# Kernel tuning notes

Measured on AMD Instinct MI355X. Metric: run time of the kernel, lower is better.

Reference implementation:

```python
import jax, jax.numpy as jnp
import numpy as np

B, NPG, C = 16, 4096, 256          # graphs, nodes per graph per type, feat dim
N = B * NPG                        # nodes per type
E = N * 16                         # edges per edge type (avg degree 16)
RATIO = 0.25
K = int(np.ceil(RATIO * NPG))      # top-k nodes per graph per type


def setup_inputs() -> dict:
    key = jax.random.key(0)
    ks = jax.random.split(key, 16)
    s = 1.0 / np.sqrt(C)
    inp = {
        "x_inst": jax.random.normal(ks[0], (N, C), jnp.float32),
        "x_data": jax.random.normal(ks[1], (N, C), jnp.float32),
        "w_kqv_inst": jax.random.normal(ks[2], (C, 3), jnp.float32) * s,
        "b_kqv_inst": jnp.zeros((3,), jnp.float32),
        "w_kqv_data": jax.random.normal(ks[3], (C, 3), jnp.float32) * s,
        "b_kqv_data": jnp.zeros((3,), jnp.float32),
        "w_out_inst": jax.random.normal(ks[4], (1, 1), jnp.float32),
        "b_out_inst": jnp.zeros((1,), jnp.float32),
        "w_out_data": jax.random.normal(ks[5], (1, 1), jnp.float32),
        "b_out_data": jnp.zeros((1,), jnp.float32),
        "krel_w": jax.random.normal(ks[6], (3,), jnp.float32),
        "krel_b": jnp.zeros((3,), jnp.float32),
        "vrel_w": jax.random.normal(ks[7], (3,), jnp.float32),
        "vrel_b": jnp.zeros((3,), jnp.float32),
        "p_rel": jnp.ones((3,), jnp.float32),
        "ei_i2d": jax.random.randint(ks[8], (2, E), 0, N, jnp.int32),
        "ei_d2i": jax.random.randint(ks[9], (2, E), 0, N, jnp.int32),
        "ei_i2i": jax.random.randint(ks[10], (2, E), 0, N, jnp.int32),
        "batch_inst": jnp.repeat(jnp.arange(B, dtype=jnp.int32), NPG),
        "batch_data": jnp.repeat(jnp.arange(B, dtype=jnp.int32), NPG),
    }
    return inp


def _hgt_scores(x_inst, x_data, w_kqv_inst, b_kqv_inst, w_kqv_data, b_kqv_data,
                w_out_inst, b_out_inst, w_out_data, b_out_data,
                krel_w, krel_b, vrel_w, vrel_b, p_rel,
                ei_i2d, ei_d2i, ei_i2i):
    # HGTConv with out_channels=1, heads=1 -> H=1, D=1 (k,q,v scalar per node)
    kqv_i = x_inst @ w_kqv_inst + b_kqv_inst   # [N,3]
    kqv_d = x_data @ w_kqv_data + b_kqv_data
    k_i, q_i, v_i = kqv_i[:, 0], kqv_i[:, 1], kqv_i[:, 2]
    k_d, q_d, v_d = kqv_d[:, 0], kqv_d[:, 1], kqv_d[:, 2]
    # dst offsets follow node-type order: inst=0, data=N
    q_glob = jnp.concatenate([q_i, q_d])       # [2N]
    Ntot = 2 * N

    def edge_terms(k_src, v_src, ei, t, dst_off):
        s, d = ei[0], ei[1]
        ke = k_src[s] * krel_w[t] + krel_b[t]  # per-relation 1x1 k_rel
        ve = v_src[s] * vrel_w[t] + vrel_b[t]  # per-relation 1x1 v_rel
        dg = d + dst_off
        logit = q_glob[dg] * ke * p_rel[t]     # (q_i*k_j).sum * p_rel / sqrt(D=1)
        return logit, ve, dg

    l0, v0, d0 = edge_terms(k_i, v_i, ei_i2d, 0, N)  # inst->data (dst=data)
    l1, v1, d1 = edge_terms(k_d, v_d, ei_d2i, 1, 0)  # data->inst (dst=inst)
    l2, v2, d2 = edge_terms(k_i, v_i, ei_i2i, 2, 0)  # inst->inst (dst=inst)
    logits = jnp.concatenate([l0, l1, l2])
    vals = jnp.concatenate([v0, v1, v2])
    dst = jnp.concatenate([d0, d1, d2])

    # segment softmax over incoming edges of each destination node
    m = jax.ops.segment_max(logits, dst, num_segments=Ntot)
    m = jnp.where(jnp.isfinite(m), m, 0.0)
    ex = jnp.exp(logits - m[dst])
    den = jax.ops.segment_sum(ex, dst, num_segments=Ntot)
    alpha = ex / den[dst]
    a = jax.ops.segment_sum(alpha * vals, dst, num_segments=Ntot)  # [2N]

    # out_lin (1->1) per node type; skip inactive (1 != 256); GELU (exact)
    s_i = jax.nn.gelu(a[:N, None] * w_out_inst[0, 0] + b_out_inst, approximate=False)
    s_d = jax.nn.gelu(a[N:, None] * w_out_data[0, 0] + b_out_data, approximate=False)
    return s_i, s_d  # [N,1] each


def _pool(x, score):
    # per-graph top-k on score, gate by tanh(score), mean over selected
    sv = score[:, 0].reshape(B, NPG)
    xv = x.reshape(B, NPG, -1)
    topv, topi = jax.lax.top_k(sv, K)                      # [B,K]
    xs = jnp.take_along_axis(xv, topi[:, :, None], axis=1)  # [B,K,C]
    return (xs * jnp.tanh(topv)[:, :, None]).mean(axis=1)   # [B,C]


def reference(x_inst, x_data, w_kqv_inst, b_kqv_inst, w_kqv_data, b_kqv_data,
              w_out_inst, b_out_inst, w_out_data, b_out_data,
              krel_w, krel_b, vrel_w, vrel_b, p_rel,
              ei_i2d, ei_d2i, ei_i2i, batch_inst, batch_data):
    # batch_* are uniform [B x NPG] blocks; pooling uses reshape equivalently.
    s_i, s_d = _hgt_scores(x_inst, x_data, w_kqv_inst, b_kqv_inst,
                           w_kqv_data, b_kqv_data, w_out_inst, b_out_inst,
                           w_out_data, b_out_data, krel_w, krel_b,
                           vrel_w, vrel_b, p_rel, ei_i2d, ei_d2i, ei_i2i)
    return jnp.concatenate([_pool(x_inst, s_i), _pool(x_data, s_d)], axis=-1)  # [B, 2C]
```

## Files before the change

### kernel.cpp

```cpp
#include <hip/hip_runtime.h>
#include <math.h>

constexpr int BB   = 16;
constexpr int NPGc = 4096;
constexpr int Cc   = 256;
constexpr int Nc   = BB * NPGc;
constexpr int Ec   = Nc * 16;
constexpr int Kc   = 1024;
constexpr int NBUK = 1024;
constexpr int BUKW = 128;
constexpr int CHUNK = 16384;
constexpr int NCHUNK = (3 * Ec) / CHUNK;

__device__ __forceinline__ unsigned long long dkey(double f) {
    long long b = __double_as_longlong(f);
    unsigned long long u = (unsigned long long)b;
    return (b < 0) ? ~u : (u | 0x8000000000000000ULL);
}
__device__ __forceinline__ double inv_dkey(unsigned long long u) {
    unsigned long long b = (u & 0x8000000000000000ULL) ? (u ^ 0x8000000000000000ULL) : ~u;
    return __longlong_as_double((long long)b);
}

__global__ __launch_bounds__(256) void kqv_kernel(
    const float* __restrict__ x_inst, const float* __restrict__ x_data,
    const float* __restrict__ w_inst, const float* __restrict__ b_inst,
    const float* __restrict__ w_data, const float* __restrict__ b_data,
    double* __restrict__ k_i, double* __restrict__ v_i,
    double* __restrict__ k_d, double* __restrict__ v_d,
    double* __restrict__ q_glob)
{
    int tid  = threadIdx.x;
    int wave = tid >> 6, lane = tid & 63;
    int grp  = lane >> 4, l = lane & 15;
    int g    = blockIdx.x * 16 + wave * 4 + grp;
    int row0 = g * 8;
    int side = (row0 >= Nc) ? 1 : 0;
    int node0 = row0 - side * Nc;
    const float* x  = side ? x_data : x_inst;
    const float* w  = side ? w_data : w_inst;
    const float* bp = side ? b_data : b_inst;

    double wr[48];
#pragma unroll
    for (int it = 0; it < 4; ++it) {
        const float4* wv = (const float4*)(w + (it * 64 + l * 4) * 3);
        float4 f0 = wv[0], f1 = wv[1], f2 = wv[2];
        float wt[12] = {f0.x, f0.y, f0.z, f0.w, f1.x, f1.y, f1.z, f1.w,
                        f2.x, f2.y, f2.z, f2.w};
#pragma unroll
        for (int e = 0; e < 12; ++e) wr[it * 12 + e] = (double)wt[e];
    }
    double b0 = (double)bp[0], b1 = (double)bp[1], b2 = (double)bp[2];

    const float4* rp = (const float4*)(x + (size_t)node0 * Cc);
#pragma unroll 2
    for (int r = 0; r < 8; ++r) {
        double kk = 0.0, qq = 0.0, vv = 0.0;
#pragma unroll
        for (int it = 0; it < 4; ++it) {
            float4 xv = rp[r * 64 + it * 16 + l];
            float xs[4] = {xv.x, xv.y, xv.z, xv.w};
#pragma unroll
            for (int u = 0; u < 4; ++u) {
                double xd = (double)xs[u];
                kk += xd * wr[it * 12 + u * 3 + 0];
                qq += xd * wr[it * 12 + u * 3 + 1];
                vv += xd * wr[it * 12 + u * 3 + 2];
            }
        }
#pragma unroll
        for (int off = 8; off; off >>= 1) {
            kk += __shfl_xor(kk, off, 64);
            qq += __shfl_xor(qq, off, 64);
            vv += __shfl_xor(vv, off, 64);
        }
        if (l == 0) {
            int node = node0 + r;
            kk += b0; qq += b1; vv += b2;
            if (side) { k_d[node] = kk; v_d[node] = vv; q_glob[Nc + node] = qq; }
            else      { k_i[node] = kk; v_i[node] = vv; q_glob[node]      = qq; }
        }
    }
}

__global__ __launch_bounds__(256) void count_kernel(
    const int* __restrict__ ei0, const int* __restrict__ ei1,
    const int* __restrict__ ei2, unsigned* __restrict__ bucket_cnt)
{
    __shared__ unsigned hist[NBUK];
    int tid = threadIdx.x;
    for (int j = tid; j < NBUK; j += 256) hist[j] = 0;
    __syncthreads();
    unsigned base = blockIdx.x * (unsigned)CHUNK;
    int t = (int)(base >> 20);
    unsigned i0 = base & (unsigned)(Ec - 1);
    const int* ei = (t == 0) ? ei0 : (t == 1) ? ei1 : ei2;
    int off = (t == 0) ? Nc : 0;
    const int4* dv = (const int4*)(ei + Ec + i0);
#pragma unroll 4
    for (int j = 0; j < CHUNK / 1024; ++j) {
        int4 d4 = dv[j * 256 + tid];
        atomicAdd(&hist[(unsigned)(d4.x + off) >> 7], 1u);
        atomicAdd(&hist[(unsigned)(d4.y + off) >> 7], 1u);
        atomicAdd(&hist[(unsigned)(d4.z + off) >> 7], 1u);
        atomicAdd(&hist[(unsigned)(d4.w + off) >> 7], 1u);
    }
    __syncthreads();
    for (int j = tid; j < NBUK; j += 256)
        if (hist[j]) atomicAdd(&bucket_cnt[j], hist[j]);
}

__global__ __launch_bounds__(1024) void scan_kernel(
    const unsigned* __restrict__ bucket_cnt,
    unsigned* __restrict__ bucket_base, unsigned* __restrict__ bucket_fill)
{
    __shared__ unsigned s[NBUK];
    int t = threadIdx.x;
    unsigned mine = bucket_cnt[t];
    s[t] = mine;
    __syncthreads();
    for (int off = 1; off < NBUK; off <<= 1) {
        unsigned v = (t >= off) ? s[t - off] : 0u;
        __syncthreads();
        s[t] += v;
        __syncthreads();
    }
    unsigned ex = s[t] - mine;
    bucket_base[t] = ex;
    bucket_fill[t] = ex;
    if (t == NBUK - 1) bucket_base[NBUK] = s[t];
}

__global__ __launch_bounds__(256) void fill_kernel(
    const int* __restrict__ ei0, const int* __restrict__ ei1,
    const int* __restrict__ ei2, unsigned* __restrict__ bucket_fill,
    unsigned* __restrict__ sorted)
{
    __shared__ unsigned hist[NBUK];
    __shared__ unsigned res[NBUK];
    int tid = threadIdx.x;
    for (int j = tid; j < NBUK; j += 256) hist[j] = 0;
    __syncthreads();
    unsigned base = blockIdx.x * (unsigned)CHUNK;
    int t = (int)(base >> 20);
    unsigned i0 = base & (unsigned)(Ec - 1);
    const int* ei = (t == 0) ? ei0 : (t == 1) ? ei1 : ei2;
    int off = (t == 0) ? Nc : 0;
    const int4* dv = (const int4*)(ei + Ec + i0);
    const int4* sv = (const int4*)(ei + i0);
#pragma unroll 4
    for (int j = 0; j < CHUNK / 1024; ++j) {
        int4 d4 = dv[j * 256 + tid];
        atomicAdd(&hist[(unsigned)(d4.x + off) >> 7], 1u);
        atomicAdd(&hist[(unsigned)(d4.y + off) >> 7], 1u);
        atomicAdd(&hist[(unsigned)(d4.z + off) >> 7], 1u);
        atomicAdd(&hist[(unsigned)(d4.w + off) >> 7], 1u);
    }
    __syncthreads();
    for (int j = tid; j < NBUK; j += 256) {
        unsigned h = hist[j];
        res[j] = h ? atomicAdd(&bucket_fill[j], h) : 0u;
        hist[j] = 0;
    }
    __syncthreads();
#pragma unroll 4
    for (int j = 0; j < CHUNK / 1024; ++j) {
        int4 d4 = dv[j * 256 + tid];
        int4 s4 = sv[j * 256 + tid];
        int dd[4] = {d4.x, d4.y, d4.z, d4.w};
        int ss[4] = {s4.x, s4.y, s4.z, s4.w};
#pragma unroll
        for (int u = 0; u < 4; ++u) {
            int dg  = dd[u] + off;
            int bkt = dg >> 7;
            unsigned local = atomicAdd(&hist[bkt], 1u);
            sorted[res[bkt] + local] =
                (unsigned)ss[u] | ((unsigned)t << 16) | ((unsigned)(dg & 127) << 18);
        }
    }
}

__global__ __launch_bounds__(256) void bucket_accum_kernel(
    const unsigned* __restrict__ bucket_base, const unsigned* __restrict__ sorted,
    const float* __restrict__ krel_w, const float* __restrict__ krel_b,
    const float* __restrict__ vrel_w, const float* __restrict__ vrel_b,
    const float* __restrict__ p_rel,
    const double* __restrict__ k_i, const double* __restrict__ v_i,
    const double* __restrict__ k_d, const double* __restrict__ v_d,
    const double* __restrict__ q_glob,
    double* __restrict__ den, double* __restrict__ num)
{
    __shared__ double den_l[BUKW];
    __shared__ double num_l[BUKW];
    __shared__ double q_l[BUKW];
    int tid = threadIdx.x;
    int b   = blockIdx.x;
    if (tid < BUKW) {
        den_l[tid] = 0.0;
        num_l[tid] = 0.0;
        q_l[tid]   = q_glob[b * BUKW + tid];
    }
    double kw0 = krel_w[0], kw1 = krel_w[1], kw2 = krel_w[2];
    double kb0 = krel_b[0], kb1 = krel_b[1], kb2 = krel_b[2];
    double vw0 = vrel_w[0], vw1 = vrel_w[1], vw2 = vrel_w[2];
    double vb0 = vrel_b[0], vb1 = vrel_b[1], vb2 = vrel_b[2];
    double pr0 = p_rel[0],  pr1 = p_rel[1],  pr2 = p_rel[2];
    unsigned beg = bucket_base[b], end = bucket_base[b + 1];
    __syncthreads();

    for (unsigned e = beg + tid; e < end; e += 256) {
        unsigned r = sorted[e];
        int s    = (int)(r & 0xFFFFu);
        int t    = (int)((r >> 16) & 3u);
        int low7 = (int)((r >> 18) & 127u);
        const double* ks = (t == 1) ? k_d : k_i;
        const double* vs = (t == 1) ? v_d : v_i;
        double kwt = (t == 0) ? kw0 : (t == 1) ? kw1 : kw2;
        double kbt = (t == 0) ? kb0 : (t == 1) ? kb1 : kb2;
        double vwt = (t == 0) ? vw0 : (t == 1) ? vw1 : vw2;
        double vbt = (t == 0) ? vb0 : (t == 1) ? vb1 : vb2;
        double prt = (t == 0) ? pr0 : (t == 1) ? pr1 : pr2;
        double ke = ks[s] * kwt + kbt;
        double ve = vs[s] * vwt + vbt;
        double ex = exp(q_l[low7] * ke * prt);
        __hip_atomic_fetch_add(&den_l[low7], ex, __ATOMIC_RELAXED,
                               __HIP_MEMORY_SCOPE_WORKGROUP);
        __hip_atomic_fetch_add(&num_l[low7], ex * ve, __ATOMIC_RELAXED,
                               __HIP_MEMORY_SCOPE_WORKGROUP);
    }
    __syncthreads();
    if (tid < BUKW) {
        den[b * BUKW + tid] = den_l[tid];
        num[b * BUKW + tid] = num_l[tid];
    }
}

__global__ __launch_bounds__(1024) void select_kernel(
    const double* __restrict__ den, const double* __restrict__ num,
    const float* __restrict__ w_out_inst, const float* __restrict__ b_out_inst,
    const float* __restrict__ w_out_data, const float* __restrict__ b_out_data,
    int* __restrict__ sel_idx, float* __restrict__ sel_w)
{
    __shared__ unsigned long long keys[NPGc];
    __shared__ unsigned hist[2048];
    __shared__ unsigned wsum[16];
    __shared__ unsigned short cand[NPGc];
    __shared__ unsigned sh_bin1, sh_rem1, sh_bin2, sh_rem2, sh_cnt, sh_nc;

    int tid  = threadIdx.x;
    int seg  = blockIdx.x;
    int side = seg >> 4;
    int b    = seg & 15;
    double wo = side ? (double)w_out_data[0] : (double)w_out_inst[0];
    double bo = side ? (double)b_out_data[0] : (double)b_out_inst[0];
    int base_node = side * Nc + b * NPGc;
    int base_sel  = seg * Kc;

    unsigned long long myk[4]; int myj[4];
#pragma unroll
    for (int p = 0; p < 4; ++p) {
        int j = p * 1024 + tid;
        double dn = den[base_node + j];
        double a  = (dn > 0.0) ? num[base_node + j] / dn : 0.0;
        double z  = a * wo + bo;
        double s  = 0.5 * z * (1.0 + erf(z * 0.7071067811865476));
        unsigned long long k64 = dkey(s);
        keys[j] = k64; myk[p] = k64; myj[p] = j;
    }
    if (tid == 0) { sh_cnt = 0; sh_nc = 0; }
    hist[tid] = 0; hist[tid + 1024] = 0;
    __syncthreads();

#pragma unroll
    for (int p = 0; p < 4; ++p) atomicAdd(&hist[(unsigned)(myk[p] >> 53)], 1u);
    __syncthreads();
    {
        unsigned g0 = hist[2047 - 2 * tid];
        unsigned g1 = hist[2046 - 2 * tid];
        unsigned x = g0 + g1;
        int lane = tid & 63;
#pragma unroll
        for (int off = 1; off < 64; off <<= 1) {
            unsigned y = __shfl_up(x, off, 64);
            if (lane >= off) x += y;
        }
        if (lane == 63) wsum[tid >> 6] = x;
        __syncthreads();
        if (tid < 16) {
            unsigned v = wsum[tid];
#pragma unroll
            for (int off = 1; off < 16; off <<= 1) {
                unsigned y = __shfl_up(v, off, 64);
                if (tid >= off) v += y;
            }
            wsum[tid] = v;
        }
        __syncthreads();
        unsigned basew = (tid >= 64) ? wsum[(tid >> 6) - 1] : 0u;
        unsigned incl  = basew + x;
        unsigned incl0 = incl - g1;
        unsigned K = Kc;
        if (incl0 >= K && incl0 - g0 < K) { sh_bin1 = 2047 - 2 * tid; sh_rem1 = K - (incl0 - g0); }
        if (incl  >= K && incl  - g1 < K) { sh_bin1 = 2046 - 2 * tid; sh_rem1 = K - (incl  - g1); }
    }
    __syncthreads();
    unsigned bin1 = sh_bin1, rem1 = sh_rem1;
    hist[tid] = 0; hist[tid + 1024] = 0;
    __syncthreads();

#pragma unroll
    for (int p = 0; p < 4; ++p)
        if ((unsigned)(myk[p] >> 53) == bin1)
            atomicAdd(&hist[(unsigned)(myk[p] >> 42) & 2047u], 1u);
    __syncthreads();
    {
        unsigned g0 = hist[2047 - 2 * tid];
        unsigned g1 = hist[2046 - 2 * tid];
        unsigned x = g0 + g1;
        int lane = tid & 63;
#pragma unroll
        for (int off = 1; off < 64; off <<= 1) {
            unsigned y = __shfl_up(x, off, 64);
            if (lane >= off) x += y;
        }
        if (lane == 63) wsum[tid >> 6] = x;
        __syncthreads();
        if (tid < 16) {
            unsigned v = wsum[tid];
#pragma unroll
            for (int off = 1; off < 16; off <<= 1) {
                unsigned y = __shfl_up(v, off, 64);
                if (tid >= off) v += y;
            }
            wsum[tid] = v;
        }
        __syncthreads();
        unsigned basew = (tid >= 64) ? wsum[(tid >> 6) - 1] : 0u;
        unsigned incl  = basew + x;
        unsigned incl0 = incl - g1;
        unsigned K = rem1;
        if (incl0 >= K && incl0 - g0 < K) { sh_bin2 = 2047 - 2 * tid; sh_rem2 = K - (incl0 - g0); }
        if (incl  >= K && incl  - g1 < K) { sh_bin2 = 2046 - 2 * tid; sh_rem2 = K - (incl  - g1); }
    }
    __syncthreads();
    unsigned long long pref22 = ((unsigned long long)bin1 << 11) | (unsigned long long)sh_bin2;
    unsigned rem2 = sh_rem2;

#pragma unroll
    for (int p = 0; p < 4; ++p) {
        unsigned long long top22 = myk[p] >> 42;
        if (top22 > pref22) {
            unsigned pos = atomicAdd(&sh_cnt, 1u);
            sel_idx[base_sel + pos] = myj[p];
            sel_w[base_sel + pos]   = (float)tanh(inv_dkey(myk[p]));
        } else if (top22 == pref22) {
            unsigned cp = atomicAdd(&sh_nc, 1u);
            cand[cp] = (unsigned short)myj[p];
        }
    }
    __syncthreads();

    unsigned nc = sh_nc;
    for (unsigned c = tid; c < nc; c += 1024) {
        int j = cand[c];
        unsigned long long k64 = keys[j];
        unsigned rank = 0;
        for (unsigned q = 0; q < nc; ++q) {
            int jq = cand[q];
            unsigned long long kq = keys[jq];
            rank += (kq > k64 || (kq == k64 && jq < j)) ? 1u : 0u;
        }
        if (rank < rem2) {
            unsigned pos = atomicAdd(&sh_cnt, 1u);
            sel_idx[base_sel + pos] = j;
            sel_w[base_sel + pos]   = (float)tanh(inv_dkey(k64));
        }
    }
}

__global__ __launch_bounds__(1024) void pool_kernel(
    const float* __restrict__ x_inst, const float* __restrict__ x_data,
    const int* __restrict__ sel_idx, const float* __restrict__ sel_w,
    float* __restrict__ out)
{
    __shared__ int   ridx[128];
    __shared__ float rw[128];
    __shared__ float accs[256];
    int tid   = threadIdx.x;
    int blk   = blockIdx.x;
    int seg   = blk >> 3;
    int chunk = blk & 7;
    int side  = seg >> 4;
    int b     = seg & 15;
    if (tid < 128) {
        ridx[tid] = sel_idx[seg * Kc + chunk * 128 + tid];
        rw[tid]   = sel_w[seg * Kc + chunk * 128 + tid];
    }
    if (tid < 256) accs[tid] = 0.0f;
    __syncthreads();
    const float* x = side ? x_data : x_inst;
    int w = tid >> 6, l = tid & 63;
    float ax = 0.f, ay = 0.f, az = 0.f, aw = 0.f;
#pragma unroll
    for (int r = 0; r < 8; ++r) {
        int   row = ridx[w * 8 + r];
        float wt  = rw[w * 8 + r];
        float4 xv = ((const float4*)(x + ((size_t)(b * NPGc + row)) * Cc))[l];
        ax += xv.x * wt; ay += xv.y * wt; az += xv.z * wt; aw += xv.w * wt;
    }
    atomicAdd(&accs[l * 4 + 0], ax);
    atomicAdd(&accs[l * 4 + 1], ay);
    atomicAdd(&accs[l * 4 + 2], az);
    atomicAdd(&accs[l * 4 + 3], aw);
    __syncthreads();
    if (tid < 256)
        unsafeAtomicAdd(&out[b * 512 + side * 256 + tid], accs[tid] * (1.0f / (float)Kc));
}

extern "C" void kernel_launch(void* const* d_in, const int* in_sizes, int n_in,
                              void* d_out, int out_size, void* d_ws, size_t ws_size,
                              hipStream_t stream) {
    const float* x_inst     = (const float*)d_in[0];
    const float* x_data     = (const float*)d_in[1];
    const float* w_kqv_inst = (const float*)d_in[2];
    const float* b_kqv_inst = (const float*)d_in[3];
    const float* w_kqv_data = (const float*)d_in[4];
    const float* b_kqv_data = (const float*)d_in[5];
    const float* w_out_inst = (const float*)d_in[6];
    const float* b_out_inst = (const float*)d_in[7];
    const float* w_out_data = (const float*)d_in[8];
    const float* b_out_data = (const float*)d_in[9];
    const float* krel_w     = (const float*)d_in[10];
    const float* krel_b     = (const float*)d_in[11];
    const float* vrel_w     = (const float*)d_in[12];
    const float* vrel_b     = (const float*)d_in[13];
    const float* p_rel      = (const float*)d_in[14];
    const int*   ei_i2d     = (const int*)d_in[15];
    const int*   ei_d2i     = (const int*)d_in[16];
    const int*   ei_i2i     = (const int*)d_in[17];
    float* out = (float*)d_out;

    char* ws = (char*)d_ws;
    double* k_i    = (double*)ws;
    double* v_i    = k_i + Nc;
    double* k_d    = v_i + Nc;
    double* v_d    = k_d + Nc;
    double* q_glob = v_d + Nc;
    double* den    = q_glob + 2 * Nc;
    double* num    = den + 2 * Nc;
    unsigned* bucket_cnt  = (unsigned*)(num + 2 * Nc);
    unsigned* bucket_base = bucket_cnt + NBUK;
    unsigned* bucket_fill = bucket_base + NBUK + 1;
    int*      sel_idx     = (int*)(bucket_fill + NBUK);
    float*    sel_w       = (float*)(sel_idx + 32 * Kc);
    unsigned* sorted      = (unsigned*)(sel_w + 32 * Kc);

    hipMemsetAsync(bucket_cnt, 0, NBUK * sizeof(unsigned), stream);
    hipMemsetAsync(d_out, 0, (size_t)out_size * sizeof(float), stream);

    count_kernel<<<NCHUNK, 256, 0, stream>>>(ei_i2d, ei_d2i, ei_i2i, bucket_cnt);
    scan_kernel<<<1, NBUK, 0, stream>>>(bucket_cnt, bucket_base, bucket_fill);
    fill_kernel<<<NCHUNK, 256, 0, stream>>>(ei_i2d, ei_d2i, ei_i2i,
                                            bucket_fill, sorted);

    kqv_kernel<<<(2 * Nc) / 128, 256, 0, stream>>>(
        x_inst, x_data, w_kqv_inst, b_kqv_inst, w_kqv_data, b_kqv_data,
        k_i, v_i, k_d, v_d, q_glob);

    bucket_accum_kernel<<<NBUK, 256, 0, stream>>>(
        bucket_base, sorted,
        krel_w, krel_b, vrel_w, vrel_b, p_rel,
        k_i, v_i, k_d, v_d, q_glob, den, num);

    select_kernel<<<32, 1024, 0, stream>>>(
        den, num, w_out_inst, b_out_inst, w_out_data, b_out_data,
        sel_idx, sel_w);

    pool_kernel<<<256, 1024, 0, stream>>>(x_inst, x_data, sel_idx, sel_w, out);
}
```

Baseline: 323.0 us.

## Switch score pipeline from double to float and retune kqv/pool grid sizes

Converts the k/q/v projection, edge softmax accumulation, and top-k selection from double to single precision. k and v are packed into one float2 per node, and fast __expf and tanhf are used. The radix select moves from 64-bit to 32-bit keys. kqv now handles 2 rows per group with all loads issued up front, and pool uses twice as many blocks. FP64 throughput and memory traffic drop, but small score differences could reorder near-tied top-k selections and the logit is clamped at 80.

After: 319.9 us. About the same (-1.0%).

```diff
diff --git a/kernel.cpp b/kernel.cpp
--- a/kernel.cpp
+++ b/kernel.cpp
@@ -12,61 +12,66 @@
 constexpr int CHUNK = 16384;
 constexpr int NCHUNK = (3 * Ec) / CHUNK;
 
-__device__ __forceinline__ unsigned long long dkey(double f) {
-    long long b = __double_as_longlong(f);
-    unsigned long long u = (unsigned long long)b;
-    return (b < 0) ? ~u : (u | 0x8000000000000000ULL);
-}
-__device__ __forceinline__ double inv_dkey(unsigned long long u) {
-    unsigned long long b = (u & 0x8000000000000000ULL) ? (u ^ 0x8000000000000000ULL) : ~u;
-    return __longlong_as_double((long long)b);
+__device__ __forceinline__ unsigned fkey(float f) {
+    int b = __float_as_int(f);
+    unsigned u = (unsigned)b;
+    return (b < 0) ? ~u : (u | 0x80000000u);
+}
+__device__ __forceinline__ float inv_fkey(unsigned u) {
+    unsigned b = (u & 0x80000000u) ? (u ^ 0x80000000u) : ~u;
+    return __int_as_float((int)b);
 }
 
 __global__ __launch_bounds__(256) void kqv_kernel(
     const float* __restrict__ x_inst, const float* __restrict__ x_data,
     const float* __restrict__ w_inst, const float* __restrict__ b_inst,
     const float* __restrict__ w_data, const float* __restrict__ b_data,
-    double* __restrict__ k_i, double* __restrict__ v_i,
-    double* __restrict__ k_d, double* __restrict__ v_d,
-    double* __restrict__ q_glob)
+    float2* __restrict__ kv_i, float2* __restrict__ kv_d,
+    float* __restrict__ q_glob)
 {
     int tid  = threadIdx.x;
     int wave = tid >> 6, lane = tid & 63;
     int grp  = lane >> 4, l = lane & 15;
     int g    = blockIdx.x * 16 + wave * 4 + grp;
-    int row0 = g * 8;
+    int row0 = g * 2;
     int side = (row0 >= Nc) ? 1 : 0;
     int node0 = row0 - side * Nc;
     const float* x  = side ? x_data : x_inst;
     const float* w  = side ? w_data : w_inst;
     const float* bp = side ? b_data : b_inst;
-
-    double wr[48];
+    float2* kv = side ? kv_d : kv_i;
+
+    float wr[48];
 #pragma unroll
     for (int it = 0; it < 4; ++it) {
         const float4* wv = (const float4*)(w + (it * 64 + l * 4) * 3);
         float4 f0 = wv[0], f1 = wv[1], f2 = wv[2];
-        float wt[12] = {f0.x, f0.y, f0.z, f0.w, f1.x, f1.y, f1.z, f1.w,
-                        f2.x, f2.y, f2.z, f2.w};
-#pragma unroll
-        for (int e = 0; e < 12; ++e) wr[it * 12 + e] = (double)wt[e];
-    }
-    double b0 = (double)bp[0], b1 = (double)bp[1], b2 = (double)bp[2];
+        wr[it*12+0]=f0.x; wr[it*12+1]=f0.y; wr[it*12+2]=f0.z; wr[it*12+3]=f0.w;
+        wr[it*12+4]=f1.x; wr[it*12+5]=f1.y; wr[it*12+6]=f1.z; wr[it*12+7]=f1.w;
+        wr[it*12+8]=f2.x; wr[it*12+9]=f2.y; wr[it*12+10]=f2.z; wr[it*12+11]=f2.w;
+    }
+    float b0 = bp[0], b1 = bp[1], b2 = bp[2];
 
     const float4* rp = (const float4*)(x + (size_t)node0 * Cc);
-#pragma unroll 2
-    for (int r = 0; r < 8; ++r) {
-        double kk = 0.0, qq = 0.0, vv = 0.0;
+    float4 xv[2][4];
+#pragma unroll
+    for (int r = 0; r < 2; ++r)
+#pragma unroll
+        for (int it = 0; it < 4; ++it)
+            xv[r][it] = rp[r * 64 + it * 16 + l];
+
+#pragma unroll
+    for (int r = 0; r < 2; ++r) {
+        float kk = 0.f, qq = 0.f, vv = 0.f;
 #pragma unroll
         for (int it = 0; it < 4; ++it) {
-            float4 xv = rp[r * 64 + it * 16 + l];
-            float xs[4] = {xv.x, xv.y, xv.z, xv.w};
+            float xs[4] = {xv[r][it].x, xv[r][it].y, xv[r][it].z, xv[r][it].w};
 #pragma unroll
             for (int u = 0; u < 4; ++u) {
-                double xd = (double)xs[u];
-                kk += xd * wr[it * 12 + u * 3 + 0];
-                qq += xd * wr[it * 12 + u * 3 + 1];
-                vv += xd * wr[it * 12 + u * 3 + 2];
+                float xd = xs[u];
+                kk = fmaf(xd, wr[it * 12 + u * 3 + 0], kk);
+                qq = fmaf(xd, wr[it * 12 + u * 3 + 1], qq);
+                vv = fmaf(xd, wr[it * 12 + u * 3 + 2], vv);
             }
         }
 #pragma unroll
@@ -77,9 +82,8 @@
         }
         if (l == 0) {
             int node = node0 + r;
-            kk += b0; qq += b1; vv += b2;
-            if (side) { k_d[node] = kk; v_d[node] = vv; q_glob[Nc + node] = qq; }
-            else      { k_i[node] = kk; v_i[node] = vv; q_glob[node]      = qq; }
+            kv[node] = make_float2(kk + b0, vv + b2);
+            q_glob[side * Nc + node] = qq + b1;
         }
     }
 }
@@ -186,26 +190,25 @@
     const float* __restrict__ krel_w, const float* __restrict__ krel_b,
     const float* __restrict__ vrel_w, const float* __restrict__ vrel_b,
     const float* __restrict__ p_rel,
-    const double* __restrict__ k_i, const double* __restrict__ v_i,
-    const double* __restrict__ k_d, const double* __restrict__ v_d,
-    const double* __restrict__ q_glob,
-    double* __restrict__ den, double* __restrict__ num)
-{
-    __shared__ double den_l[BUKW];
-    __shared__ double num_l[BUKW];
-    __shared__ double q_l[BUKW];
+    const float2* __restrict__ kv_i, const float2* __restrict__ kv_d,
+    const float* __restrict__ q_glob,
+    float* __restrict__ den, float* __restrict__ num)
+{
+    __shared__ float den_l[BUKW];
+    __shared__ float num_l[BUKW];
+    __shared__ float q_l[BUKW];
     int tid = threadIdx.x;
     int b   = blockIdx.x;
     if (tid < BUKW) {
-        den_l[tid] = 0.0;
-        num_l[tid] = 0.0;
+        den_l[tid] = 0.0f;
+        num_l[tid] = 0.0f;
         q_l[tid]   = q_glob[b * BUKW + tid];
     }
-    double kw0 = krel_w[0], kw1 = krel_w[1], kw2 = krel_w[2];
-    double kb0 = krel_b[0], kb1 = krel_b[1], kb2 = krel_b[2];
-    double vw0 = vrel_w[0], vw1 = vrel_w[1], vw2 = vrel_w[2];
-    double vb0 = vrel_b[0], vb1 = vrel_b[1], vb2 = vrel_b[2];
-    double pr0 = p_rel[0],  pr1 = p_rel[1],  pr2 = p_rel[2];
+    float kw0 = krel_w[0], kw1 = krel_w[1], kw2 = krel_w[2];
+    float kb0 = krel_b[0], kb1 = krel_b[1], kb2 = krel_b[2];
+    float vw0 = vrel_w[0], vw1 = vrel_w[1], vw2 = vrel_w[2];
+    float vb0 = vrel_b[0], vb1 = vrel_b[1], vb2 = vrel_b[2];
+    float pr0 = p_rel[0],  pr1 = p_rel[1],  pr2 = p_rel[2];
     unsigned beg = bucket_base[b], end = bucket_base[b + 1];
     __syncthreads();
 
@@ -214,16 +217,16 @@
         int s    = (int)(r & 0xFFFFu);
         int t    = (int)((r >> 16) & 3u);
         int low7 = (int)((r >> 18) & 127u);
-        const double* ks = (t == 1) ? k_d : k_i;
-        const double* vs = (t == 1) ? v_d : v_i;
-        double kwt = (t == 0) ? kw0 : (t == 1) ? kw1 : kw2;
-        double kbt = (t == 0) ? kb0 : (t == 1) ? kb1 : kb2;
-        double vwt = (t == 0) ? vw0 : (t == 1) ? vw1 : vw2;
-        double vbt = (t == 0) ? vb0 : (t == 1) ? vb1 : vb2;
-        double prt = (t == 0) ? pr0 : (t == 1) ? pr1 : pr2;
-        double ke = ks[s] * kwt + kbt;
-        double ve = vs[s] * vwt + vbt;
-        double ex = exp(q_l[low7] * ke * prt);
+        float2 kvv = (t == 1) ? kv_d[s] : kv_i[s];
+        float kwt = (t == 0) ? kw0 : (t == 1) ? kw1 : kw2;
+        float kbt = (t == 0) ? kb0 : (t == 1) ? kb1 : kb2;
+        float vwt = (t == 0) ? vw0 : (t == 1) ? vw1 : vw2;
+        float vbt = (t == 0) ? vb0 : (t == 1) ? vb1 : vb2;
+        float prt = (t == 0) ? pr0 : (t == 1) ? pr1 : pr2;
+        float ke = fmaf(kvv.x, kwt, kbt);
+        float ve = fmaf(kvv.y, vwt, vbt);
+        float logit = q_l[low7] * ke * prt;
+        float ex = __expf(fminf(logit, 80.0f));
         __hip_atomic_fetch_add(&den_l[low7], ex, __ATOMIC_RELAXED,
                                __HIP_MEMORY_SCOPE_WORKGROUP);
         __hip_atomic_fetch_add(&num_l[low7], ex * ve, __ATOMIC_RELAXED,
@@ -237,12 +240,12 @@
 }
 
 __global__ __launch_bounds__(1024) void select_kernel(
-    const double* __restrict__ den, const double* __restrict__ num,
+    const float* __restrict__ den, const float* __restrict__ num,
     const float* __restrict__ w_out_inst, const float* __restrict__ b_out_inst,
     const float* __restrict__ w_out_data, const float* __restrict__ b_out_data,
     int* __restrict__ sel_idx, float* __restrict__ sel_w)
 {
-    __shared__ unsigned long long keys[NPGc];
+    __shared__ unsigned keys[NPGc];
     __shared__ unsigned hist[2048];
     __shared__ unsigned wsum[16];
     __shared__ unsigned short cand[NPGc];
@@ -252,28 +255,28 @@
     int seg  = blockIdx.x;
     int side = seg >> 4;
     int b    = seg & 15;
-    double wo = side ? (double)w_out_data[0] : (double)w_out_inst[0];
-    double bo = side ? (double)b_out_data[0] : (double)b_out_inst[0];
+    float wo = side ? w_out_data[0] : w_out_inst[0];
+    float bo = side ? b_out_data[0] : b_out_inst[0];
     int base_node = side * Nc + b * NPGc;
     int base_sel  = seg * Kc;
 
-    unsigned long long myk[4]; int myj[4];
+    unsigned myk[4]; int myj[4];
 #pragma unroll
     for (int p = 0; p < 4; ++p) {
         int j = p * 1024 + tid;
-        double dn = den[base_node + j];
-        double a  = (dn > 0.0) ? num[base_node + j] / dn : 0.0;
-        double z  = a * wo + bo;
-        double s  = 0.5 * z * (1.0 + erf(z * 0.7071067811865476));
-        unsigned long long k64 = dkey(s);
-        keys[j] = k64; myk[p] = k64; myj[p] = j;
+        float dn = den[base_node + j];
+        float a  = (dn > 0.0f) ? num[base_node + j] / dn : 0.0f;
+        float z  = fmaf(a, wo, bo);
+        float s  = 0.5f * z * (1.0f + erff(z * 0.70710678f));
+        unsigned k32 = fkey(s);
+        keys[j] = k32; myk[p] = k32; myj[p] = j;
     }
     if (tid == 0) { sh_cnt = 0; sh_nc = 0; }
     hist[tid] = 0; hist[tid + 1024] = 0;
     __syncthreads();
 
 #pragma unroll
-    for (int p = 0; p < 4; ++p) atomicAdd(&hist[(unsigned)(myk[p] >> 53)], 1u);
+    for (int p = 0; p < 4; ++p) atomicAdd(&hist[myk[p] >> 21], 1u);
     __syncthreads();
     {
         unsigned g0 = hist[2047 - 2 * tid];
@@ -302,7 +305,7 @@
         unsigned incl0 = incl - g1;
         unsigned K = Kc;
         if (incl0 >= K && incl0 - g0 < K) { sh_bin1 = 2047 - 2 * tid; sh_rem1 = K - (incl0 - g0); }
-        if (incl  >= K && incl  - g1 < K) { sh_bin1 = 2046 - 2 * tid; sh_rem1 = K - (incl  - g1); }
+        if (incl  >= K && incl0     < K) { sh_bin1 = 2046 - 2 * tid; sh_rem1 = K - incl0; }
     }
     __syncthreads();
     unsigned bin1 = sh_bin1, rem1 = sh_rem1;
@@ -311,8 +314,8 @@
 
 #pragma unroll
     for (int p = 0; p < 4; ++p)
-        if ((unsigned)(myk[p] >> 53) == bin1)
-            atomicAdd(&hist[(unsigned)(myk[p] >> 42) & 2047u], 1u);
+        if ((myk[p] >> 21) == bin1)
+            atomicAdd(&hist[(myk[p] >> 10) & 2047u], 1u);
     __syncthreads();
     {
         unsigned g0 = hist[2047 - 2 * tid];
@@ -341,19 +344,19 @@
         unsigned incl0 = incl - g1;
         unsigned K = rem1;
         if (incl0 >= K && incl0 - g0 < K) { sh_bin2 = 2047 - 2 * tid; sh_rem2 = K - (incl0 - g0); }
-        if (incl  >= K && incl  - g1 < K) { sh_bin2 = 2046 - 2 * tid; sh_rem2 = K - (incl  - g1); }
-    }
-    __syncthreads();
-    unsigned long long pref22 = ((unsigned long long)bin1 << 11) | (unsigned long long)sh_bin2;
+        if (incl  >= K && incl0     < K) { sh_bin2 = 2046 - 2 * tid; sh_rem2 = K - incl0; }
+    }
+    __syncthreads();
+    unsigned pref22 = (bin1 << 11) | sh_bin2;
     unsigned rem2 = sh_rem2;
 
 #pragma unroll
     for (int p = 0; p < 4; ++p) {
-        unsigned long long top22 = myk[p] >> 42;
+        unsigned top22 = myk[p] >> 10;
         if (top22 > pref22) {
             unsigned pos = atomicAdd(&sh_cnt, 1u);
             sel_idx[base_sel + pos] = myj[p];
-            sel_w[base_sel + pos]   = (float)tanh(inv_dkey(myk[p]));
+            sel_w[base_sel + pos]   = tanhf(inv_fkey(myk[p]));
         } else if (top22 == pref22) {
             unsigned cp = atomicAdd(&sh_nc, 1u);
             cand[cp] = (unsigned short)myj[p];
@@ -364,17 +367,17 @@
     unsigned nc = sh_nc;
     for (unsigned c = tid; c < nc; c += 1024) {
         int j = cand[c];
-        unsigned long long k64 = keys[j];
+        unsigned k32 = keys[j];
         unsigned rank = 0;
         for (unsigned q = 0; q < nc; ++q) {
             int jq = cand[q];
-            unsigned long long kq = keys[jq];
-            rank += (kq > k64 || (kq == k64 && jq < j)) ? 1u : 0u;
+            unsigned kq = keys[jq];
+            rank += (kq > k32 || (kq == k32 && jq < j)) ? 1u : 0u;
         }
         if (rank < rem2) {
             unsigned pos = atomicAdd(&sh_cnt, 1u);
             sel_idx[base_sel + pos] = j;
-            sel_w[base_sel + pos]   = (float)tanh(inv_dkey(k64));
+            sel_w[base_sel + pos]   = tanhf(inv_fkey(k32));
         }
     }
 }
@@ -384,18 +387,18 @@
     const int* __restrict__ sel_idx, const float* __restrict__ sel_w,
     float* __restrict__ out)
 {
-    __shared__ int   ridx[128];
-    __shared__ float rw[128];
+    __shared__ int   ridx[64];
+    __shared__ float rw[64];
     __shared__ float accs[256];
     int tid   = threadIdx.x;
     int blk   = blockIdx.x;
-    int seg   = blk >> 3;
-    int chunk = blk & 7;
+    int seg   = blk >> 4;
+    int chunk = blk & 15;
     int side  = seg >> 4;
     int b     = seg & 15;
-    if (tid < 128) {
-        ridx[tid] = sel_idx[seg * Kc + chunk * 128 + tid];
-        rw[tid]   = sel_w[seg * Kc + chunk * 128 + tid];
+    if (tid < 64) {
+        ridx[tid] = sel_idx[seg * Kc + chunk * 64 + tid];
+        rw[tid]   = sel_w[seg * Kc + chunk * 64 + tid];
     }
     if (tid < 256) accs[tid] = 0.0f;
     __syncthreads();
@@ -403,11 +406,12 @@
     int w = tid >> 6, l = tid & 63;
     float ax = 0.f, ay = 0.f, az = 0.f, aw = 0.f;
 #pragma unroll
-    for (int r = 0; r < 8; ++r) {
-        int   row = ridx[w * 8 + r];
-        float wt  = rw[w * 8 + r];
+    for (int r = 0; r < 4; ++r) {
+        int   row = ridx[w * 4 + r];
+        float wt  = rw[w * 4 + r];
         float4 xv = ((const float4*)(x + ((size_t)(b * NPGc + row)) * Cc))[l];
-        ax += xv.x * wt; ay += xv.y * wt; az += xv.z * wt; aw += xv.w * wt;
+        ax = fmaf(xv.x, wt, ax); ay = fmaf(xv.y, wt, ay);
+        az = fmaf(xv.z, wt, az); aw = fmaf(xv.w, wt, aw);
     }
     atomicAdd(&accs[l * 4 + 0], ax);
     atomicAdd(&accs[l * 4 + 1], ay);
@@ -442,13 +446,11 @@
     float* out = (float*)d_out;
 
     char* ws = (char*)d_ws;
-    double* k_i    = (double*)ws;
-    double* v_i    = k_i + Nc;
-    double* k_d    = v_i + Nc;
-    double* v_d    = k_d + Nc;
-    double* q_glob = v_d + Nc;
-    double* den    = q_glob + 2 * Nc;
-    double* num    = den + 2 * Nc;
+    float2* kv_i   = (float2*)ws;
+    float2* kv_d   = kv_i + Nc;
+    float*  q_glob = (float*)(kv_d + Nc);
+    float*  den    = q_glob + 2 * Nc;
+    float*  num    = den + 2 * Nc;
     unsigned* bucket_cnt  = (unsigned*)(num + 2 * Nc);
     unsigned* bucket_base = bucket_cnt + NBUK;
     unsigned* bucket_fill = bucket_base + NBUK + 1;
@@ -464,18 +466,18 @@
     fill_kernel<<<NCHUNK, 256, 0, stream>>>(ei_i2d, ei_d2i, ei_i2i,
                                             bucket_fill, sorted);
 
-    kqv_kernel<<<(2 * Nc) / 128, 256, 0, stream>>>(
+    kqv_kernel<<<(2 * Nc) / 32, 256, 0, stream>>>(
         x_inst, x_data, w_kqv_inst, b_kqv_inst, w_kqv_data, b_kqv_data,
-        k_i, v_i, k_d, v_d, q_glob);
+        kv_i, kv_d, q_glob);
 
     bucket_accum_kernel<<<NBUK, 256, 0, stream>>>(
         bucket_base, sorted,
         krel_w, krel_b, vrel_w, vrel_b, p_rel,
-        k_i, v_i, k_d, v_d, q_glob, den, num);
+        kv_i, kv_d, q_glob, den, num);
 
     select_kernel<<<32, 1024, 0, stream>>>(
         den, num, w_out_inst, b_out_inst, w_out_data, b_out_data,
         sel_idx, sel_w);
 
-    pool_kernel<<<256, 1024, 0, stream>>>(x_inst, x_data, sel_idx, sel_w, out);
-}
+    pool_kernel<<<512, 1024, 0, stream>>>(x_inst, x_data, sel_idx, sel_w, out);
+}
```
